# Optimization experiments

Hardware: AMD Instinct MI355X
Metric: run time of the kernel (lower is better)

The kernel has to match this reference:

```python
import jax, jax.numpy as jnp
import numpy as np

B, S, D = 2, 2048, 1024
H, DH = 16, 64  # num_heads, per-head depth (kd//H == vd//H)
NEG = -1e10


def setup_inputs() -> dict:
    key = jax.random.key(0)
    ks = jax.random.split(key, 5)
    scale = 0.02
    return {
        "X": jax.random.normal(ks[0], (B, S, D), dtype=jnp.float32),
        "Wq": jax.random.normal(ks[1], (D, D), dtype=jnp.float32) * scale,
        "Wk": jax.random.normal(ks[2], (D, D), dtype=jnp.float32) * scale,
        "Wv": jax.random.normal(ks[3], (D, D), dtype=jnp.float32) * scale,
        "Wo": jax.random.normal(ks[4], (D, D), dtype=jnp.float32) * scale,
    }


def reference(X, Wq, Wk, Wv, Wo):
    # torch nn.Linear(in,out,bias=False): y = x @ W.T, W is [out,in]
    q = X @ Wq.T  # [B,S,H*DH]
    k = X @ Wk.T
    v = X @ Wv.T
    # split heads -> [B,H,S,DH]
    q = q.reshape(B, S, H, DH).transpose(0, 2, 1, 3) * (DH ** -0.5)
    k = k.reshape(B, S, H, DH).transpose(0, 2, 1, 3)
    v = v.reshape(B, S, H, DH).transpose(0, 2, 1, 3)
    # causal bias: -1e10 on strictly upper triangle (psuedolikelihood=False)
    bias = NEG * jnp.triu(jnp.ones((S, S), dtype=jnp.float32), 1)
    # logits[...,q,k] = q . k
    logits = jnp.einsum("bhkd,bhqd->bhqk", k, q) + bias
    weights = jax.nn.softmax(logits, axis=-1)  # [B,H,S,S]
    out = jnp.einsum("bhqk,bhkd->bhqd", weights, v)
    out = out.transpose(0, 2, 1, 3).reshape(B, S, H * DH)
    return out @ Wo.T  # [B,S,D]
```

## Files before the change

### kernel.cpp

```cpp
#include <hip/hip_runtime.h>
#include <math.h>


typedef _Float16 f16x8 __attribute__((ext_vector_type(8)));
typedef _Float16 f16x4 __attribute__((ext_vector_type(4)));
typedef _Float16 f16x2 __attribute__((ext_vector_type(2)));
typedef __attribute__((ext_vector_type(4))) float f32x4;
typedef __attribute__((ext_vector_type(16))) float f32x16;

#define MFMA16(a, b, c) __builtin_amdgcn_mfma_f32_16x16x32_f16(a, b, c, 0, 0, 0)
#define MFMA32(a, b, c) __builtin_amdgcn_mfma_f32_32x32x16_f16(a, b, c, 0, 0, 0)
#define QSCALE 0.18033688f

__device__ __forceinline__ f16x2 pk2(float x, float y) {
  return __builtin_bit_cast(f16x2, __builtin_amdgcn_cvt_pkrtz(x, y));
}

__device__ __forceinline__ f16x8 cvt8(const float* __restrict__ p) {
  float4 a = *(const float4*)p;
  float4 b = *(const float4*)(p + 4);
  f16x2 p0 = pk2(a.x, a.y), p1 = pk2(a.z, a.w);
  f16x2 p2 = pk2(b.x, b.y), p3 = pk2(b.z, b.w);
  f16x8 h;
  h[0] = p0[0]; h[1] = p0[1]; h[2] = p1[0]; h[3] = p1[1];
  h[4] = p2[0]; h[5] = p2[1]; h[6] = p3[0]; h[7] = p3[1];
  return h;
}

__global__ void convert_all(const float* __restrict__ X, const float* __restrict__ Wq,
                            const float* __restrict__ Wk, const float* __restrict__ Wv,
                            const float* __restrict__ Wo, _Float16* __restrict__ Xh,
                            _Float16* __restrict__ Wqkvh, _Float16* __restrict__ Woh) {
  size_t i = ((size_t)blockIdx.x * 256 + threadIdx.x) * 8;
  const float* src; _Float16* dst; size_t off;
  if (i < 4194304u)      { src = X;  dst = Xh;              off = i; }
  else if (i < 5242880u) { src = Wq; dst = Wqkvh;           off = i - 4194304u; }
  else if (i < 6291456u) { src = Wk; dst = Wqkvh + 1048576; off = i - 5242880u; }
  else if (i < 7340032u) { src = Wv; dst = Wqkvh + 2097152; off = i - 6291456u; }
  else                   { src = Wo; dst = Woh;             off = i - 7340032u; }
  *(f16x8*)(dst + off) = cvt8(src + off);
}

template <int BH>
__global__ __launch_bounds__(256) void gemm_qkv(
    const _Float16* __restrict__ Xh, const float* __restrict__ Wq,
    const float* __restrict__ Wk, const float* __restrict__ Wv,
    const _Float16* __restrict__ Wh, _Float16* __restrict__ Qh,
    _Float16* __restrict__ Kh, _Float16* __restrict__ Vth) {
  __shared__ _Float16 As[128 * 72];
  __shared__ _Float16 Bs[128 * 72];
  const int tid = threadIdx.x;
  const int wave = tid >> 6, lane = tid & 63;
  const int quad = lane >> 4, l16 = lane & 15;
  const int wm = (wave >> 1) * 64, wn = (wave & 1) * 64;
  const int bn = blockIdx.x, bm = blockIdx.y;
  const int mat = bn >> 3;
  const float* Bsrc = (mat == 0) ? Wq : (mat == 1) ? Wk : Wv;
  const int brow0 = (bn & 7) * 128;

  f32x4 acc[4][4] = {};

  for (int k0 = 0; k0 < 1024; k0 += 64) {
    __syncthreads();
#pragma unroll
    for (int j = 0; j < 4; ++j) {
      int idx = tid + j * 256;
      int row = idx >> 3, c8 = idx & 7;
      *(int4*)&As[row * 72 + c8 * 8] =
          *(const int4*)&Xh[(size_t)(bm * 128 + row) * 1024 + k0 + c8 * 8];
      if (BH)
        *(int4*)&Bs[row * 72 + c8 * 8] =
            *(const int4*)&Wh[(size_t)(bn * 128 + row) * 1024 + k0 + c8 * 8];
      else
        *(f16x8*)&Bs[row * 72 + c8 * 8] =
            cvt8(&Bsrc[(size_t)(brow0 + row) * 1024 + k0 + c8 * 8]);
    }
    __syncthreads();
#pragma unroll
    for (int kc = 0; kc < 2; ++kc) {
      f16x8 af[4], bf[4];
#pragma unroll
      for (int t = 0; t < 4; ++t) {
        af[t] = *(const f16x8*)&As[(wm + t * 16 + l16) * 72 + kc * 32 + quad * 8];
        bf[t] = *(const f16x8*)&Bs[(wn + t * 16 + l16) * 72 + kc * 32 + quad * 8];
      }
#pragma unroll
      for (int mt = 0; mt < 4; ++mt)
#pragma unroll
        for (int nt = 0; nt < 4; ++nt)
          acc[mt][nt] = MFMA16(af[mt], bf[nt], acc[mt][nt]);
    }
  }

#pragma unroll
  for (int mt = 0; mt < 4; ++mt) {
    int m_base = bm * 128 + wm + mt * 16 + quad * 4;
    int b = m_base >> 11, sb = m_base & 2047;
#pragma unroll
    for (int nt = 0; nt < 4; ++nt) {
      int ob = (bn * 128 + wn + nt * 16) & 1023;
      int h = ob >> 6;
      int dh = (ob & 63) + l16;
      size_t bh = (size_t)(b * 16 + h);
      if (mat == 0) {
#pragma unroll
        for (int r = 0; r < 4; ++r)
          Qh[(bh * 2048 + sb + r) * 64 + dh] = (_Float16)(acc[mt][nt][r] * QSCALE);
      } else if (mat == 1) {
#pragma unroll
        for (int r = 0; r < 4; ++r)
          Kh[(bh * 2048 + sb + r) * 64 + dh] = (_Float16)acc[mt][nt][r];
      } else {
        f16x4 pk;
        pk[0] = (_Float16)acc[mt][nt][0];
        pk[1] = (_Float16)acc[mt][nt][1];
        pk[2] = (_Float16)acc[mt][nt][2];
        pk[3] = (_Float16)acc[mt][nt][3];
        *(f16x4*)&Vth[(bh * 64 + dh) * 2048 + sb] = pk;
      }
    }
  }
}

__global__ __launch_bounds__(256) void attn_kernel(
    const _Float16* __restrict__ Qg, const _Float16* __restrict__ Kg,
    const _Float16* __restrict__ Vtg, _Float16* __restrict__ Og) {
  __shared__ _Float16 Kl[128 * 72];
  __shared__ _Float16 Vl[64 * 136];
  const int bh = blockIdx.x;
  const int qt = 15 - (int)blockIdx.y;
  const int q0 = qt * 128;
  const int tid = threadIdx.x;
  const int wave = tid >> 6, lane = tid & 63;
  const int l31 = lane & 31, hl = lane >> 5;
  const int b = bh >> 4, h = bh & 15;
  const int qrow = q0 + wave * 32 + l31;

  const _Float16* Qbase =
      Qg + ((size_t)bh * 2048 + qrow) * 64 + hl * 8;
  f16x8 aq[4];
#pragma unroll
  for (int t = 0; t < 4; ++t) aq[t] = *(const f16x8*)(Qbase + 16 * t);

  f32x16 oacc[2] = {};
  float lsum = 0.f;

  const int ktiles = qt + 1;
  for (int kt = 0; kt < ktiles; ++kt) {
    const int k0 = kt << 7;
    __syncthreads();
#pragma unroll
    for (int i = tid; i < 1024; i += 256) {
      int row = i >> 3, c8 = i & 7;
      *(int4*)&Kl[row * 72 + c8 * 8] =
          *(const int4*)&Kg[((size_t)bh * 2048 + k0 + row) * 64 + c8 * 8];
    }
#pragma unroll
    for (int i = tid; i < 1024; i += 256) {
      int row = i >> 4, c16 = i & 15;
      *(int4*)&Vl[row * 136 + c16 * 8] =
          *(const int4*)&Vtg[((size_t)bh * 64 + row) * 2048 + k0 + c16 * 8];
    }
    __syncthreads();

    const bool diag = (kt == ktiles - 1);

#pragma unroll
    for (int s32t = 0; s32t < 4; ++s32t) {
      f32x16 tv = {};
#pragma unroll
      for (int t = 0; t < 4; ++t) {
        f16x8 kb = *(const f16x8*)&Kl[(s32t * 32 + l31) * 72 + t * 16 + hl * 8];
        tv = MFMA32(kb, aq[t], tv);
      }
      int pkx[8];
#pragma unroll
      for (int i = 0; i < 8; ++i) {
        float x0 = tv[2 * i], x1 = tv[2 * i + 1];
        int kg = k0 + s32t * 32 + ((2 * i) & 3) + 8 * (i >> 1) + 4 * hl;
        if (diag) {
          if (kg > qrow) x0 = -1e30f;
          if (kg + 1 > qrow) x1 = -1e30f;
        }
        x0 = __builtin_amdgcn_exp2f(x0);
        x1 = __builtin_amdgcn_exp2f(x1);
        lsum += x0 + x1;
        pkx[i] = __builtin_bit_cast(int, pk2(x0, x1));
      }
      int s0 = hl ? pkx[0] : pkx[2];
      int s1 = hl ? pkx[1] : pkx[3];
      int s2 = hl ? pkx[4] : pkx[6];
      int s3 = hl ? pkx[5] : pkx[7];
      int r0 = __shfl_xor(s0, 32);
      int r1 = __shfl_xor(s1, 32);
      int r2 = __shfl_xor(s2, 32);
      int r3 = __shfl_xor(s3, 32);
      int4 f0, f1;
      f0.x = hl ? r0 : pkx[0];
      f0.y = hl ? r1 : pkx[1];
      f0.z = hl ? pkx[2] : r0;
      f0.w = hl ? pkx[3] : r1;
      f1.x = hl ? r2 : pkx[4];
      f1.y = hl ? r3 : pkx[5];
      f1.z = hl ? pkx[6] : r2;
      f1.w = hl ? pkx[7] : r3;
      f16x8 bp0 = __builtin_bit_cast(f16x8, f0);
      f16x8 bp1 = __builtin_bit_cast(f16x8, f1);
#pragma unroll
      for (int d = 0; d < 2; ++d) {
        f16x8 vb0 = *(const f16x8*)&Vl[(d * 32 + l31) * 136 + s32t * 32 + hl * 8];
        f16x8 vb1 =
            *(const f16x8*)&Vl[(d * 32 + l31) * 136 + s32t * 32 + 16 + hl * 8];
        oacc[d] = MFMA32(vb0, bp0, oacc[d]);
        oacc[d] = MFMA32(vb1, bp1, oacc[d]);
      }
    }
  }

  lsum += __shfl_xor(lsum, 32);
  float inv = 1.0f / lsum;
#pragma unroll
  for (int d = 0; d < 2; ++d)
#pragma unroll
    for (int rq = 0; rq < 4; ++rq) {
      f16x4 o;
#pragma unroll
      for (int j = 0; j < 4; ++j)
        o[j] = (_Float16)(oacc[d][rq * 4 + j] * inv);
      int dh = d * 32 + 8 * rq + 4 * hl;
      *(f16x4*)&Og[(((size_t)b * 2048 + qrow) * 16 + h) * 64 + dh] = o;
    }
}

template <int BH>
__global__ __launch_bounds__(256) void gemm_out(
    const _Float16* __restrict__ A, const float* __restrict__ Wo,
    const _Float16* __restrict__ Woh, float* __restrict__ Co) {
  __shared__ _Float16 As[128 * 72];
  __shared__ _Float16 Bs[64 * 72];
  const int tid = threadIdx.x;
  const int wave = tid >> 6, lane = tid & 63;
  const int quad = lane >> 4, l16 = lane & 15;
  const int wm = (wave >> 1) * 64, wn = (wave & 1) * 32;
  const int bn = blockIdx.x, bm = blockIdx.y;

  f32x4 acc[4][2] = {};

  for (int k0 = 0; k0 < 1024; k0 += 64) {
    __syncthreads();
#pragma unroll
    for (int j = 0; j < 4; ++j) {
      int idx = tid + j * 256;
      int row = idx >> 3, c8 = idx & 7;
      *(int4*)&As[row * 72 + c8 * 8] =
          *(const int4*)&A[(size_t)(bm * 128 + row) * 1024 + k0 + c8 * 8];
    }
#pragma unroll
    for (int j = 0; j < 2; ++j) {
      int idx = tid + j * 256;
      int row = idx >> 3, c8 = idx & 7;
      if (BH)
        *(int4*)&Bs[row * 72 + c8 * 8] =
            *(const int4*)&Woh[(size_t)(bn * 64 + row) * 1024 + k0 + c8 * 8];
      else
        *(f16x8*)&Bs[row * 72 + c8 * 8] =
            cvt8(&Wo[(size_t)(bn * 64 + row) * 1024 + k0 + c8 * 8]);
    }
    __syncthreads();
#pragma unroll
    for (int kc = 0; kc < 2; ++kc) {
      f16x8 af[4], bf[2];
#pragma unroll
      for (int t = 0; t < 4; ++t)
        af[t] = *(const f16x8*)&As[(wm + t * 16 + l16) * 72 + kc * 32 + quad * 8];
#pragma unroll
      for (int t = 0; t < 2; ++t)
        bf[t] = *(const f16x8*)&Bs[(wn + t * 16 + l16) * 72 + kc * 32 + quad * 8];
#pragma unroll
      for (int mt = 0; mt < 4; ++mt)
#pragma unroll
        for (int nt = 0; nt < 2; ++nt)
          acc[mt][nt] = MFMA16(af[mt], bf[nt], acc[mt][nt]);
    }
  }

#pragma unroll
  for (int mt = 0; mt < 4; ++mt) {
    int m_base = bm * 128 + wm + mt * 16 + quad * 4;
#pragma unroll
    for (int nt = 0; nt < 2; ++nt) {
      int n = bn * 64 + wn + nt * 16 + l16;
#pragma unroll
      for (int r = 0; r < 4; ++r)
        Co[(size_t)(m_base + r) * 1024 + n] = acc[mt][nt][r];
    }
  }
}

extern "C" void kernel_launch(void* const* d_in, const int* in_sizes, int n_in,
                              void* d_out, int out_size, void* d_ws, size_t ws_size,
                              hipStream_t stream) {
  const float* X  = (const float*)d_in[0];
  const float* Wq = (const float*)d_in[1];
  const float* Wk = (const float*)d_in[2];
  const float* Wv = (const float*)d_in[3];
  const float* Wo = (const float*)d_in[4];
  float* out = (float*)d_out;

  _Float16* Qh    = (_Float16*)d_out;
  _Float16* Kh    = Qh + 4194304;
  _Float16* Vth   = (_Float16*)d_ws;
  _Float16* Xh    = Vth + 4194304;
  _Float16* Og    = Xh;
  _Float16* Wqkvh = Xh + 4194304;
  _Float16* Woh   = Wqkvh + 3145728;

  const bool big = (ws_size >= 25165824u);

  convert_all<<<big ? 4096 : 2048, 256, 0, stream>>>(X, Wq, Wk, Wv, Wo,
                                                     Xh, Wqkvh, Woh);
  if (big)
    gemm_qkv<1><<<dim3(24, 32), 256, 0, stream>>>(Xh, Wq, Wk, Wv, Wqkvh,
                                                  Qh, Kh, Vth);
  else
    gemm_qkv<0><<<dim3(24, 32), 256, 0, stream>>>(Xh, Wq, Wk, Wv, nullptr,
                                                  Qh, Kh, Vth);
  attn_kernel<<<dim3(32, 16), 256, 0, stream>>>(Qh, Kh, Vth, Og);
  if (big)
    gemm_out<1><<<dim3(16, 32), 256, 0, stream>>>(Og, Wo, Woh, out);
  else
    gemm_out<0><<<dim3(16, 32), 256, 0, stream>>>(Og, Wo, nullptr, out);
}
```

Measured before the change: 212.5 us.

## Split attention KV tiles across two wave groups and merge partial outputs

Doubles the attention block to 512 threads. The two 256-thread groups process alternating key tiles of the causal range, each with its own shared-memory K/V buffer, and their partial accumulators and sums are combined through shared memory at the end. The goal is to roughly halve the serial key loop per block, so the long diagonal-heavy tiles get more parallelism and better latency hiding. In exchange it uses twice the LDS and registers per block, adds a reduction step, and leaves one group idle on odd tile counts. The softmax uses no running max, so summing the partial results needs no rescaling.

```diff
diff --git a/kernel.cpp b/kernel.cpp
--- a/kernel.cpp
+++ b/kernel.cpp
@@ -122,22 +122,26 @@
   }
 }
 
-__global__ __launch_bounds__(256) void attn_kernel(
+__global__ __launch_bounds__(512) void attn_kernel(
     const _Float16* __restrict__ Qg, const _Float16* __restrict__ Kg,
     const _Float16* __restrict__ Vtg, _Float16* __restrict__ Og) {
-  __shared__ _Float16 Kl[128 * 72];
-  __shared__ _Float16 Vl[64 * 136];
+  __shared__ _Float16 smem[2 * (128 * 72 + 64 * 136)];
   const int bh = blockIdx.x;
   const int qt = 15 - (int)blockIdx.y;
   const int q0 = qt * 128;
   const int tid = threadIdx.x;
-  const int wave = tid >> 6, lane = tid & 63;
+  const int group = tid >> 8;
+  const int tidg = tid & 255;
+  const int wv = (tid >> 6) & 3;
+  const int lane = tid & 63;
   const int l31 = lane & 31, hl = lane >> 5;
   const int b = bh >> 4, h = bh & 15;
-  const int qrow = q0 + wave * 32 + l31;
-
-  const _Float16* Qbase =
-      Qg + ((size_t)bh * 2048 + qrow) * 64 + hl * 8;
+  const int qrow = q0 + wv * 32 + l31;
+
+  _Float16* Kl = smem + group * (128 * 72 + 64 * 136);
+  _Float16* Vl = Kl + 128 * 72;
+
+  const _Float16* Qbase = Qg + ((size_t)bh * 2048 + qrow) * 64 + hl * 8;
   f16x8 aq[4];
 #pragma unroll
   for (int t = 0; t < 4; ++t) aq[t] = *(const f16x8*)(Qbase + 16 * t);
@@ -145,25 +149,30 @@
   f32x16 oacc[2] = {};
   float lsum = 0.f;
 
-  const int ktiles = qt + 1;
-  for (int kt = 0; kt < ktiles; ++kt) {
+  const int nmax = (qt + 2) >> 1;
+  for (int it = 0; it < nmax; ++it) {
+    const int kt = 2 * it + group;
+    const bool valid = (kt <= qt);
     const int k0 = kt << 7;
     __syncthreads();
-#pragma unroll
-    for (int i = tid; i < 1024; i += 256) {
-      int row = i >> 3, c8 = i & 7;
-      *(int4*)&Kl[row * 72 + c8 * 8] =
-          *(const int4*)&Kg[((size_t)bh * 2048 + k0 + row) * 64 + c8 * 8];
-    }
-#pragma unroll
-    for (int i = tid; i < 1024; i += 256) {
-      int row = i >> 4, c16 = i & 15;
-      *(int4*)&Vl[row * 136 + c16 * 8] =
-          *(const int4*)&Vtg[((size_t)bh * 64 + row) * 2048 + k0 + c16 * 8];
-    }
-    __syncthreads();
-
-    const bool diag = (kt == ktiles - 1);
+    if (valid) {
+#pragma unroll
+      for (int i = tidg; i < 1024; i += 256) {
+        int row = i >> 3, c8 = i & 7;
+        *(int4*)&Kl[row * 72 + c8 * 8] =
+            *(const int4*)&Kg[((size_t)bh * 2048 + k0 + row) * 64 + c8 * 8];
+      }
+#pragma unroll
+      for (int i = tidg; i < 1024; i += 256) {
+        int row = i >> 4, c16 = i & 15;
+        *(int4*)&Vl[row * 136 + c16 * 8] =
+            *(const int4*)&Vtg[((size_t)bh * 64 + row) * 2048 + k0 + c16 * 8];
+      }
+    }
+    __syncthreads();
+    if (!valid) continue;
+
+    const bool diag = (kt == qt);
 
 #pragma unroll
     for (int s32t = 0; s32t < 4; ++s32t) {
@@ -217,19 +226,37 @@
     }
   }
 
-  lsum += __shfl_xor(lsum, 32);
-  float inv = 1.0f / lsum;
-#pragma unroll
-  for (int d = 0; d < 2; ++d)
-#pragma unroll
-    for (int rq = 0; rq < 4; ++rq) {
-      f16x4 o;
-#pragma unroll
-      for (int j = 0; j < 4; ++j)
-        o[j] = (_Float16)(oacc[d][rq * 4 + j] * inv);
-      int dh = d * 32 + 8 * rq + 4 * hl;
-      *(f16x4*)&Og[(((size_t)b * 2048 + qrow) * 16 + h) * 64 + dh] = o;
-    }
+  __syncthreads();
+  float* mbuf = (float*)(smem + (128 * 72 + 64 * 136));
+  float* slot = mbuf + (wv * 64 + lane) * 33;
+  if (group == 1) {
+#pragma unroll
+    for (int d = 0; d < 2; ++d)
+#pragma unroll
+      for (int j = 0; j < 16; ++j) slot[d * 16 + j] = oacc[d][j];
+    slot[32] = lsum;
+  }
+  __syncthreads();
+  if (group == 0) {
+#pragma unroll
+    for (int d = 0; d < 2; ++d)
+#pragma unroll
+      for (int j = 0; j < 16; ++j) oacc[d][j] += slot[d * 16 + j];
+    lsum += slot[32];
+    lsum += __shfl_xor(lsum, 32);
+    float inv = 1.0f / lsum;
+#pragma unroll
+    for (int d = 0; d < 2; ++d)
+#pragma unroll
+      for (int rq = 0; rq < 4; ++rq) {
+        f16x4 o;
+#pragma unroll
+        for (int j = 0; j < 4; ++j)
+          o[j] = (_Float16)(oacc[d][rq * 4 + j] * inv);
+        int dh = d * 32 + 8 * rq + 4 * hl;
+        *(f16x4*)&Og[(((size_t)b * 2048 + qrow) * 16 + h) * 64 + dh] = o;
+      }
+  }
 }
 
 template <int BH>
@@ -325,7 +352,7 @@
   else
     gemm_qkv<0><<<dim3(24, 32), 256, 0, stream>>>(Xh, Wq, Wk, Wv, nullptr,
                                                   Qh, Kh, Vth);
-  attn_kernel<<<dim3(32, 16), 256, 0, stream>>>(Qh, Kh, Vth, Og);
+  attn_kernel<<<dim3(32, 16), 512, 0, stream>>>(Qh, Kh, Vth, Og);
   if (big)
     gemm_out<1><<<dim3(16, 32), 256, 0, stream>>>(Og, Wo, Woh, out);
   else
```

After: 184.2 us. 13.3% less time.
